# Kernel optimization log

Hardware: AMD Instinct MI355X
Metric: run time of the kernel (lower is better)

The kernel has to match this reference:

```python
import jax, jax.numpy as jnp
import numpy as np

N0, N1 = 4096, 16384
HID, LAT, DIM, OUT = 128, 64, 3, 3
OFFS = [1, 2, 3, 5, 8]  # circulant graph offsets; A+A^3 support is offset sums


def _ring_edges(N, offs):
    # edge_index of A + A^3 for circulant adjacency with given offsets
    o = np.asarray(offs)
    s3 = (o[:, None, None] + o[None, :, None] + o[None, None, :]).ravel()
    aug = np.unique(np.concatenate([o, s3]))
    src = np.repeat(np.arange(N), aug.size)
    dst = (src + np.tile(aug, N)) % N
    return np.stack([src, dst]).astype(np.int32)


def _gatv2(x, src, dst, eattr, Wl, bl, Wr, br, We, att, bias, N):
    # PyG GATv2Conv, heads=1, add_self_loops=True with fill_value='mean'
    cnt = jax.ops.segment_sum(jnp.ones_like(dst, jnp.float32), dst, N)
    loop_attr = jax.ops.segment_sum(eattr, dst, N) / jnp.maximum(cnt, 1.0)[:, None]
    loops = jnp.arange(N, dtype=src.dtype)
    s = jnp.concatenate([src, loops])
    d = jnp.concatenate([dst, loops])
    ea = jnp.concatenate([eattr, loop_attr], 0)
    xl = x @ Wl.T + bl
    xr = x @ Wr.T + br
    m = xl[s] + xr[d] + ea @ We.T              # [E+N, HID]
    m = jnp.where(m > 0, m, 0.2 * m)           # leaky_relu(0.2)
    a = m @ att                                # [E+N]
    amax = jax.ops.segment_max(a, d, N)
    ex = jnp.exp(a - amax[d])
    den = jax.ops.segment_sum(ex, d, N)
    alpha = ex / (den[d] + 1e-16)
    return jax.ops.segment_sum(xl[s] * alpha[:, None], d, N) + bias


def _knn_interp(x, pos_x, pos_y, k=3):
    # PyG knn_interpolate: inverse-squared-distance weighted k-NN average
    d2 = (jnp.sum(pos_y ** 2, 1)[:, None] + jnp.sum(pos_x ** 2, 1)[None, :]
          - 2.0 * pos_y @ pos_x.T)             # [Ny, Nx]
    neg, idx = jax.lax.top_k(-d2, k)
    w = 1.0 / jnp.maximum(-neg, 1e-16)          # [Ny, k]
    return jnp.sum(x[idx] * w[..., None], 1) / jnp.sum(w, 1)[:, None]


def _forward(latent, pos0, pos1, eidx0, eidx1, conv_Wl, conv_bl, conv_Wr,
             conv_br, conv_We, conv_att, conv_bias, lin0_W, lin0_b, lins_W,
             lins_b, out_W, out_b):
    x = latent @ lin0_W.T + lin0_b
    src0, dst0 = eidx0[0], eidx0[1]
    ea0 = pos0[dst0] - pos0[src0]
    for c in (0, 1):
        h = jnp.concatenate([x, pos0], 1)
        x = jax.nn.elu(_gatv2(h, src0, dst0, ea0, conv_Wl[c], conv_bl[c],
                              conv_Wr[c], conv_br[c], conv_We[c], conv_att[c],
                              conv_bias[c], N0)) + h @ lins_W[c].T + lins_b[c]
    x = _knn_interp(x, pos0, pos1, 3)
    src1, dst1 = eidx1[0], eidx1[1]
    ea1 = pos1[dst1] - pos1[src1]
    for c in (2, 3):
        h = jnp.concatenate([x, pos1], 1)
        x = jax.nn.elu(_gatv2(h, src1, dst1, ea1, conv_Wl[c], conv_bl[c],
                              conv_Wr[c], conv_br[c], conv_We[c], conv_att[c],
                              conv_bias[c], N1)) + h @ lins_W[c].T + lins_b[c]
    h = jnp.concatenate([x, pos1], 1)
    return h @ out_W.T + out_b


def setup_inputs() -> dict:
    key = jax.random.key(0)
    ks = jax.random.split(key, 16)
    n = lambda i, shape, s=0.05: jax.random.normal(ks[i], shape, jnp.float32) * s
    IN = HID + DIM
    return dict(
        latent=jax.random.normal(ks[0], (N0, LAT), jnp.float32),
        pos0=jax.random.normal(ks[1], (N0, DIM), jnp.float32),
        pos1=jax.random.normal(ks[2], (N1, DIM), jnp.float32),
        eidx0=jnp.asarray(_ring_edges(N0, OFFS)),
        eidx1=jnp.asarray(_ring_edges(N1, OFFS)),
        conv_Wl=n(3, (4, HID, IN)), conv_bl=n(4, (4, HID)),
        conv_Wr=n(5, (4, HID, IN)), conv_br=n(6, (4, HID)),
        conv_We=n(7, (4, HID, DIM)), conv_att=n(8, (4, HID)),
        conv_bias=n(9, (4, HID)),
        lin0_W=n(10, (HID, LAT)), lin0_b=n(11, (HID,)),
        lins_W=n(12, (4, HID, IN)), lins_b=n(13, (4, HID)),
        out_W=n(14, (OUT, IN)), out_b=n(15, (OUT,)))


def reference(latent, pos0, pos1, eidx0, eidx1, conv_Wl, conv_bl, conv_Wr,
              conv_br, conv_We, conv_att, conv_bias, lin0_W, lin0_b, lins_W,
              lins_b, out_W, out_b):
    return _forward(latent, pos0, pos1, eidx0, eidx1, conv_Wl, conv_bl,
                    conv_Wr, conv_br, conv_We, conv_att, conv_bias, lin0_W,
                    lin0_b, lins_W, lins_b, out_W, out_b)
```

## Files before the change

### kernel.cpp

```cpp
#include <hip/hip_runtime.h>
#include <hip/hip_bf16.h>

#define N0 4096
#define N1 16384
#define HID 128
#define LAT 64
#define DIM 3
#define NAUG 21
#define JTOT 512
#define NG 5

typedef __attribute__((ext_vector_type(8))) short bf16x8;
typedef __attribute__((ext_vector_type(4))) float f32x4;

__device__ __constant__ int c_aug[NAUG] = {1,2,3,4,5,6,7,8,9,10,11,12,13,14,
                                           15,16,17,18,19,21,24};

__device__ __forceinline__ unsigned short f2bf(float v) {
    __hip_bfloat16 b = __float2bfloat16(v);
    return *reinterpret_cast<unsigned short*>(&b);
}

#define KCH 64
#define KCS 64
#define YPT 4
#define KNN_BLOCKS 1024

#define WSWZ_PER_LAYER 81920
#define H0G4 131072
#define H1G4 524288
#define P_NSWZ (4 * WSWZ_PER_LAYER)
#define P_B0 P_NSWZ
#define P_B1 (P_B0 + 4 * JTOT)
#define P_B2 (P_B1 + H0G4)
#define P_B3 (P_B2 + H1G4)
#define PREP_BLOCKS (P_B3 / 256)
#define LIN0_BLOCKS 2048

__global__ __launch_bounds__(256)
void prep_knn_lin0_kernel(const float* __restrict__ Wl,
                          const float* __restrict__ Wr,
                          const float* __restrict__ We,
                          const float* __restrict__ linsW,
                          const float* __restrict__ bl,
                          const float* __restrict__ br,
                          const float* __restrict__ linsb,
                          const float* __restrict__ lin0W,
                          const float* __restrict__ lin0b,
                          const float* __restrict__ latent,
                          const float* __restrict__ pos0,
                          const float* __restrict__ pos1,
                          unsigned short* __restrict__ Wswz,
                          float* __restrict__ bias_cat,
                          unsigned short* __restrict__ hswz0A,
                          unsigned short* __restrict__ hswz0B,
                          unsigned short* __restrict__ hswz1A,
                          unsigned short* __restrict__ hswz1B,
                          float* __restrict__ pb_d,
                          int* __restrict__ pb_i) {
    __shared__ float4 sx[KCS];

    if (blockIdx.x < KNN_BLOCKS) {
        int tid = threadIdx.x;
        int chunk = blockIdx.x >> 4;
        int xpart = blockIdx.x & 15;
        if (tid < KCS) {
            const float* p = &pos0[(chunk * KCS + tid) * 3];
            float x = p[0], y = p[1], z = p[2];
            sx[tid] = make_float4(x, y, z, x * x + y * y + z * z);
        }
        __syncthreads();
        int ybase = xpart * (256 * YPT) + tid;
        float m2y[YPT][3], sy[YPT];
#pragma unroll
        for (int u = 0; u < YPT; ++u) {
            int y = ybase + u * 256;
            float p0 = pos1[y * 3], p1 = pos1[y * 3 + 1], p2 = pos1[y * 3 + 2];
            m2y[u][0] = -2.0f * p0; m2y[u][1] = -2.0f * p1; m2y[u][2] = -2.0f * p2;
            sy[u] = p0 * p0 + p1 * p1 + p2 * p2;
        }
        float bd0[YPT], bd1[YPT], bd2[YPT];
        int   bi0[YPT], bi1[YPT], bi2[YPT];
#pragma unroll
        for (int u = 0; u < YPT; ++u) {
            bd0[u] = 1e30f; bd1[u] = 1e30f; bd2[u] = 1e30f;
            bi0[u] = 0; bi1[u] = 0; bi2[u] = 0;
        }
        int gbase = chunk * KCS;
#pragma unroll 4
        for (int i = 0; i < KCS; i += 4) {
            float4 s[4];
#pragma unroll
            for (int v = 0; v < 4; ++v) s[v] = sx[i + v];
#pragma unroll
            for (int v = 0; v < 4; ++v) {
                int gi = gbase + i + v;
#pragma unroll
                for (int u = 0; u < YPT; ++u) {
                    float t = fmaf(m2y[u][0], s[v].x, s[v].w);
                    t = fmaf(m2y[u][1], s[v].y, t);
                    t = fmaf(m2y[u][2], s[v].z, t);
                    t += sy[u];
                    bool c0 = t < bd0[u];
                    bool c1 = t < bd1[u];
                    bool c2 = t < bd2[u];
                    float n0 = fminf(bd0[u], t);
                    float n1 = __builtin_amdgcn_fmed3f(bd0[u], bd1[u], t);
                    float n2 = __builtin_amdgcn_fmed3f(bd1[u], bd2[u], t);
                    int j0 = c0 ? gi : bi0[u];
                    int j1 = c0 ? bi0[u] : (c1 ? gi : bi1[u]);
                    int j2 = c1 ? bi1[u] : (c2 ? gi : bi2[u]);
                    bd0[u] = n0; bd1[u] = n1; bd2[u] = n2;
                    bi0[u] = j0; bi1[u] = j1; bi2[u] = j2;
                }
            }
        }
#pragma unroll
        for (int u = 0; u < YPT; ++u) {
            int y = ybase + u * 256;
            int base = (chunk * N1 + y) * 3;
            pb_d[base] = bd0[u]; pb_d[base + 1] = bd1[u]; pb_d[base + 2] = bd2[u];
            pb_i[base] = bi0[u]; pb_i[base + 1] = bi1[u]; pb_i[base + 2] = bi2[u];
        }
        return;
    }

    if (blockIdx.x < KNN_BLOCKS + PREP_BLOCKS) {
        int tid = (blockIdx.x - KNN_BLOCKS) * blockDim.x + threadIdx.x;
        if (tid < P_NSWZ) {
            int c = tid / WSWZ_PER_LAYER;
            int r = tid - c * WSWZ_PER_LAYER;
            int nt = r / 2560;
            int g  = (r / 512) % 5;
            int l  = (r / 8) % 64;
            int j  = r % 8;
            int k  = g * 32 + (l >> 4) * 8 + j;
            int n  = nt * 16 + (l & 15);
            float v = 0.0f;
            if (k < 131) {
                if (n < 128)      v = Wl[(c * 128 + n) * 131 + k];
                else if (n < 256) v = Wr[(c * 128 + (n - 128)) * 131 + k];
                else if (n < 384) v = linsW[(c * 128 + (n - 256)) * 131 + k];
                else              v = (k >= 128) ? We[(c * 128 + (n - 384)) * 3 + (k - 128)]
                                                 : 0.0f;
            }
            Wswz[tid] = f2bf(v);
        } else if (tid < P_B1) {
            int idx = tid - P_B0;
            int c = idx / JTOT;
            int j = idx - c * JTOT;
            float v;
            if (j < 128)        v = bl[c * 128 + j];
            else if (j < 256)   v = br[c * 128 + (j - 128)];
            else if (j < 384)   v = linsb[c * 128 + (j - 256)];
            else                v = 0.0f;
            bias_cat[idx] = v;
        } else if (tid < P_B2) {
            int r = tid - P_B1;
            int j = r & 7;
            int l = (r >> 3) & 63;
            int mt = r >> 9;
            int row = mt * 16 + (l & 15);
            int k = 128 + (l >> 4) * 8 + j;
            float v = (k < 131) ? pos0[row * 3 + (k - 128)] : 0.0f;
            unsigned short bv = f2bf(v);
            size_t idx = (size_t)((mt * 5 + 4) * 64 + l) * 8 + j;
            hswz0A[idx] = bv;
            hswz0B[idx] = bv;
        } else if (tid < P_B3) {
            int r = tid - P_B2;
            int j = r & 7;
            int l = (r >> 3) & 63;
            int mt = r >> 9;
            int row = mt * 16 + (l & 15);
            int k = 128 + (l >> 4) * 8 + j;
            float v = (k < 131) ? pos1[row * 3 + (k - 128)] : 0.0f;
            unsigned short bv = f2bf(v);
            size_t idx = (size_t)((mt * 5 + 4) * 64 + l) * 8 + j;
            hswz1A[idx] = bv;
            hswz1B[idx] = bv;
        }
        return;
    }

    {
        int r = (blockIdx.x - KNN_BLOCKS - PREP_BLOCKS) * blockDim.x + threadIdx.x;
        int n = r >> 7, j = r & 127;
        const float* lr = &latent[n * 64];
        const float* wr = &lin0W[j * 64];
        float acc = lin0b[j];
#pragma unroll 8
        for (int k = 0; k < 64; ++k) acc += lr[k] * wr[k];
        int g = j >> 5, sub = (j >> 3) & 3, jj = j & 7;
        hswz0A[(size_t)(((n >> 4) * 5 + g) * 64 + sub * 16 + (n & 15)) * 8 + jj] = f2bf(acc);
    }
}

#define WROW 40
#define FSTR 132

__device__ __forceinline__ void layer_body(
        const unsigned short* __restrict__ hswz,
        const unsigned short* __restrict__ Wswz,
        const float* __restrict__ bias_cat,
        const float* __restrict__ att,
        const float* __restrict__ bias,
        float* __restrict__ linb,
        float* __restrict__ xout,
        unsigned short* __restrict__ hout,
        const float* __restrict__ outW,
        const float* __restrict__ outb,
        const float* __restrict__ pos1,
        int mode, int N, int mt0,
        float (*xls_s)[FSTR], float (*pes_s)[FSTR], float (*xr_s)[FSTR]) {
    int tid = threadIdx.x;
    int w = tid >> 6;
    int l = tid & 63;
    int quad = l >> 4, lcol = l & 15;
    int n0 = mt0 * 16;
    int MT = N >> 4;

    bf16x8 a[3][NG];
#pragma unroll
    for (int i = 0; i < 3; ++i) {
        int mt = mt0 - 2 + i;
        if (mt < 0) mt += MT;
#pragma unroll
        for (int g = 0; g < NG; ++g)
            a[i][g] = *(const bf16x8*)&hswz[(size_t)((mt * NG + g) * 64 + l) * 8];
    }

#pragma unroll
    for (int i = 0; i < 4; ++i) {
        int b = i * 8 + w;
        int colbase = (b & 7) * 16;
        int ntw, kind;
        if (b < 8)       { ntw = b;      kind = 0; }
        else if (b < 16) { ntw = 16 + b; kind = 1; }
        else if (b < 24) { ntw = b - 8;  kind = 2; }
        else             { ntw = b - 8;  kind = 3; }
        bf16x8 bf[NG];
#pragma unroll
        for (int g = 0; g < NG; ++g)
            bf[g] = *(const bf16x8*)&Wswz[(size_t)((ntw * NG + g) * 64 + l) * 8];
        float bv = bias_cat[ntw * 16 + lcol];
        if (kind < 2) {
            float (*dst)[FSTR] = (kind == 0) ? xls_s : pes_s;
#pragma unroll
            for (int m = 0; m < 3; ++m) {
                f32x4 c = {bv, bv, bv, bv};
#pragma unroll
                for (int g = 0; g < NG; ++g)
                    c = __builtin_amdgcn_mfma_f32_16x16x32_bf16(a[m][g], bf[g], c, 0, 0, 0);
                if (m == 0) {
                    if (quad >= 2) {
                        int w0 = (quad - 2) * 4;
#pragma unroll
                        for (int r = 0; r < 4; ++r) dst[w0 + r][colbase + lcol] = c[r];
                    }
                } else {
                    int w0 = m * 16 - 8 + quad * 4;
#pragma unroll
                    for (int r = 0; r < 4; ++r) dst[w0 + r][colbase + lcol] = c[r];
                }
            }
        } else if (kind == 2) {
            f32x4 c = {bv, bv, bv, bv};
#pragma unroll
            for (int g = 0; g < NG; ++g)
                c = __builtin_amdgcn_mfma_f32_16x16x32_bf16(a[2][g], bf[g], c, 0, 0, 0);
            int w0 = quad * 4;
#pragma unroll
            for (int r = 0; r < 4; ++r) xr_s[w0 + r][colbase + lcol] = c[r];
        } else {
            f32x4 c = {bv, bv, bv, bv};
#pragma unroll
            for (int g = 0; g < NG; ++g)
                c = __builtin_amdgcn_mfma_f32_16x16x32_bf16(a[2][g], bf[g], c, 0, 0, 0);
            int jj = colbase + lcol;
#pragma unroll
            for (int r = 0; r < 4; ++r)
                linb[(size_t)(n0 + quad * 4 + r) * 128 + jj] = c[r];
        }
    }
    __syncthreads();

    int qh = l >> 5;
    int t = l & 31;
    int dl = w * 2 + qh;
    int d = n0 + dl;
    int selfrow = dl + 24;
    int i0 = t * 4;

    f32x4 linv = *(const f32x4*)&linb[(size_t)d * 128 + i0];

    float att4[4], base[4], xld[4], pesum[4], o[4];
    {
        f32x4 a0 = *(const f32x4*)&att[i0];
        f32x4 r0 = *(const f32x4*)&xr_s[dl][i0];
        f32x4 x0 = *(const f32x4*)&xls_s[selfrow][i0];
        f32x4 p0 = *(const f32x4*)&pes_s[selfrow][i0];
#pragma unroll
        for (int j = 0; j < 4; ++j) {
            att4[j] = a0[j];
            xld[j]  = x0[j];
            base[j] = r0[j] + p0[j];
            pesum[j] = 0.0f;
            o[j] = 0.0f;
        }
    }

    float den = 0.0f;

#pragma unroll
    for (int k = 0; k < NAUG; ++k) {
        int lr = selfrow - c_aug[k];
        float xls[4], pes[4];
        *(f32x4*)&xls[0] = *(const f32x4*)&xls_s[lr][i0];
        *(f32x4*)&pes[0] = *(const f32x4*)&pes_s[lr][i0];
        float p = 0.0f;
#pragma unroll
        for (int j = 0; j < 4; ++j) {
            float mm = xls[j] + base[j] - pes[j];
            mm = mm > 0.0f ? mm : 0.2f * mm;
            p = fmaf(att4[j], mm, p);
            pesum[j] += pes[j];
        }
        p += __shfl_xor(p, 1, 64);
        p += __shfl_xor(p, 2, 64);
        p += __shfl_xor(p, 4, 64);
        p += __shfl_xor(p, 8, 64);
        p += __shfl_xor(p, 16, 64);
        float wgt = __expf(p);
        den += wgt;
#pragma unroll
        for (int j = 0; j < 4; ++j) o[j] = fmaf(wgt, xls[j], o[j]);
    }
    {
        const float inv21 = 1.0f / 21.0f;
        float p = 0.0f;
#pragma unroll
        for (int j = 0; j < 4; ++j) {
            float mm = xld[j] + base[j] - pesum[j] * inv21;
            mm = mm > 0.0f ? mm : 0.2f * mm;
            p = fmaf(att4[j], mm, p);
        }
        p += __shfl_xor(p, 1, 64);
        p += __shfl_xor(p, 2, 64);
        p += __shfl_xor(p, 4, 64);
        p += __shfl_xor(p, 8, 64);
        p += __shfl_xor(p, 16, 64);
        float wgt = __expf(p);
        den += wgt;
#pragma unroll
        for (int j = 0; j < 4; ++j) o[j] = fmaf(wgt, xld[j], o[j]);
    }

    float inv = 1.0f / (den + 1e-16f);
    float res[4];
    {
        f32x4 b0 = *(const f32x4*)&bias[i0];
#pragma unroll
        for (int j = 0; j < 4; ++j) {
            float v = o[j] * inv + b0[j];
            v = v > 0.0f ? v : __expf(v) - 1.0f;
            res[j] = v + linv[j];
        }
    }

    if (mode == 0) {
        *(f32x4*)&xout[(size_t)d * 128 + i0] = *(f32x4*)&res[0];
    } else if (mode == 1) {
        unsigned short ob[4];
#pragma unroll
        for (int j = 0; j < 4; ++j) ob[j] = f2bf(res[j]);
        int g = i0 >> 5, sub = (i0 >> 3) & 3, jj = i0 & 7;
        *(uint2*)&hout[(size_t)((((d >> 4) * 5 + g) * 64) + sub * 16 + (d & 15)) * 8 + jj]
            = *(uint2*)ob;
    } else {
        float po[3];
#pragma unroll
        for (int o3 = 0; o3 < 3; ++o3) {
            const float* wr = &outW[o3 * 131 + i0];
            float p = res[0] * wr[0];
            p = fmaf(res[1], wr[1], p);
            p = fmaf(res[2], wr[2], p);
            p = fmaf(res[3], wr[3], p);
            p += __shfl_xor(p, 1, 64);
            p += __shfl_xor(p, 2, 64);
            p += __shfl_xor(p, 4, 64);
            p += __shfl_xor(p, 8, 64);
            p += __shfl_xor(p, 16, 64);
            po[o3] = p;
        }
        if (t == 0) {
            float p0 = pos1[d * 3], p1 = pos1[d * 3 + 1], p2 = pos1[d * 3 + 2];
#pragma unroll
            for (int o3 = 0; o3 < 3; ++o3) {
                xout[d * 3 + o3] = po[o3] + outb[o3] + p0 * outW[o3 * 131 + 128]
                                 + p1 * outW[o3 * 131 + 129] + p2 * outW[o3 * 131 + 130];
            }
        }
    }
}

__global__ __launch_bounds__(512, 2)
void fused_layer_kernel(const unsigned short* __restrict__ hswz,
                        const unsigned short* __restrict__ Wswz,
                        const float* __restrict__ bias_cat,
                        const float* __restrict__ att,
                        const float* __restrict__ bias,
                        float* __restrict__ linb,
                        float* __restrict__ xout,
                        unsigned short* __restrict__ hout,
                        const float* __restrict__ outW,
                        const float* __restrict__ outb,
                        const float* __restrict__ pos1,
                        int mode, int N) {
    __shared__ __align__(16) float xls_s[WROW][FSTR];
    __shared__ __align__(16) float pes_s[WROW][FSTR];
    __shared__ __align__(16) float xr_s[16][FSTR];
    layer_body(hswz, Wswz, bias_cat, att, bias, linb, xout, hout,
               outW, outb, pos1, mode, N, blockIdx.x, xls_s, pes_s, xr_s);
}

#define MERGE_BLOCKS 32

__global__ __launch_bounds__(512, 2)
void layer0_merge_kernel(const unsigned short* __restrict__ hswz,
                         const unsigned short* __restrict__ Wswz,
                         const float* __restrict__ bias_cat,
                         const float* __restrict__ att,
                         const float* __restrict__ bias,
                         float* __restrict__ linb,
                         unsigned short* __restrict__ hout,
                         const float* __restrict__ pb_d,
                         const int* __restrict__ pb_i,
                         int* __restrict__ knn_idx,
                         float* __restrict__ knn_w) {
    __shared__ __align__(16) float xls_s[WROW][FSTR];
    __shared__ __align__(16) float pes_s[WROW][FSTR];
    __shared__ __align__(16) float xr_s[16][FSTR];

    if (blockIdx.x < (N0 >> 4)) {
        layer_body(hswz, Wswz, bias_cat, att, bias, linb, nullptr, hout,
                   nullptr, nullptr, nullptr, 1, N0, blockIdx.x,
                   xls_s, pes_s, xr_s);
        return;
    }

    int y = (blockIdx.x - (N0 >> 4)) * 512 + threadIdx.x;
    float bd0 = 1e30f, bd1 = 1e30f, bd2 = 1e30f;
    int bi0 = 0, bi1 = 0, bi2 = 0;
    for (int c = 0; c < KCH; ++c) {
        int base = (c * N1 + y) * 3;
#pragma unroll
        for (int t3 = 0; t3 < 3; ++t3) {
            float t = pb_d[base + t3];
            int gi = pb_i[base + t3];
            bool c0 = t < bd0;
            bool c1 = t < bd1;
            bool c2 = t < bd2;
            float n0 = fminf(bd0, t);
            float n1 = __builtin_amdgcn_fmed3f(bd0, bd1, t);
            float n2 = __builtin_amdgcn_fmed3f(bd1, bd2, t);
            int j0 = c0 ? gi : bi0;
            int j1 = c0 ? bi0 : (c1 ? gi : bi1);
            int j2 = c1 ? bi1 : (c2 ? gi : bi2);
            bd0 = n0; bd1 = n1; bd2 = n2;
            bi0 = j0; bi1 = j1; bi2 = j2;
        }
    }
    knn_idx[y * 3]     = bi0;
    knn_idx[y * 3 + 1] = bi1;
    knn_idx[y * 3 + 2] = bi2;
    knn_w[y * 3]     = 1.0f / fmaxf(bd0, 1e-16f);
    knn_w[y * 3 + 1] = 1.0f / fmaxf(bd1, 1e-16f);
    knn_w[y * 3 + 2] = 1.0f / fmaxf(bd2, 1e-16f);
}

__global__ __launch_bounds__(256)
void interp_kernel(const float* __restrict__ x0, const int* __restrict__ knn_idx,
                   const float* __restrict__ knn_w, unsigned short* __restrict__ hswz) {
    int wave = threadIdx.x >> 6;
    int lane = threadIdx.x & 63;
    int y = blockIdx.x * 4 + wave;
    int i0 = 2 * lane;
    float w0 = knn_w[y * 3], w1 = knn_w[y * 3 + 1], w2 = knn_w[y * 3 + 2];
    int j0 = knn_idx[y * 3], j1 = knn_idx[y * 3 + 1], j2 = knn_idx[y * 3 + 2];
    float inv = 1.0f / (w0 + w1 + w2);
    float2 a = *(const float2*)&x0[(size_t)j0 * 128 + i0];
    float2 b = *(const float2*)&x0[(size_t)j1 * 128 + i0];
    float2 c = *(const float2*)&x0[(size_t)j2 * 128 + i0];
    float rx = (w0 * a.x + w1 * b.x + w2 * c.x) * inv;
    float ry = (w0 * a.y + w1 * b.y + w2 * c.y) * inv;
    unsigned int packed = (unsigned int)f2bf(rx) | ((unsigned int)f2bf(ry) << 16);
    int g = i0 >> 5, sub = (i0 >> 3) & 3, jj = i0 & 7;
    size_t idx = (size_t)((((y >> 4) * 5 + g) * 64) + sub * 16 + (y & 15)) * 8 + jj;
    *(unsigned int*)&hswz[idx] = packed;
}

extern "C" void kernel_launch(void* const* d_in, const int* in_sizes, int n_in,
                              void* d_out, int out_size, void* d_ws, size_t ws_size,
                              hipStream_t stream) {
    (void)in_sizes; (void)n_in; (void)out_size; (void)ws_size;
    const float* latent   = (const float*)d_in[0];
    const float* pos0     = (const float*)d_in[1];
    const float* pos1     = (const float*)d_in[2];
    const float* conv_Wl  = (const float*)d_in[5];
    const float* conv_bl  = (const float*)d_in[6];
    const float* conv_Wr  = (const float*)d_in[7];
    const float* conv_br  = (const float*)d_in[8];
    const float* conv_We  = (const float*)d_in[9];
    const float* conv_att = (const float*)d_in[10];
    const float* conv_bias= (const float*)d_in[11];
    const float* lin0_W   = (const float*)d_in[12];
    const float* lin0_b   = (const float*)d_in[13];
    const float* lins_W   = (const float*)d_in[14];
    const float* lins_b   = (const float*)d_in[15];
    const float* out_W    = (const float*)d_in[16];
    const float* out_b    = (const float*)d_in[17];
    float* out = (float*)d_out;

    char* ws = (char*)d_ws;
    unsigned short* Wswz = (unsigned short*)ws; ws += (size_t)4 * WSWZ_PER_LAYER * 2;
    float* bias_cat = (float*)ws;  ws += (size_t)4 * JTOT * 4;
    unsigned short* hswz0A = (unsigned short*)ws; ws += (size_t)(N0 / 16) * NG * 64 * 8 * 2;
    unsigned short* hswz0B = (unsigned short*)ws; ws += (size_t)(N0 / 16) * NG * 64 * 8 * 2;
    unsigned short* hswz1A = (unsigned short*)ws; ws += (size_t)(N1 / 16) * NG * 64 * 8 * 2;
    unsigned short* hswz1B = (unsigned short*)ws; ws += (size_t)(N1 / 16) * NG * 64 * 8 * 2;
    float* bufA     = (float*)ws;  ws += (size_t)N0 * 128 * 4;
    float* linb     = (float*)ws;  ws += (size_t)N1 * 128 * 4;
    float* pb_d     = (float*)ws;  ws += (size_t)KCH * N1 * 3 * 4;
    int*   pb_i     = (int*)ws;    ws += (size_t)KCH * N1 * 3 * 4;
    int*   knn_idx  = (int*)ws;    ws += (size_t)N1 * 3 * 4;
    float* knn_w    = (float*)ws;  ws += (size_t)N1 * 3 * 4;

    prep_knn_lin0_kernel<<<KNN_BLOCKS + PREP_BLOCKS + LIN0_BLOCKS, 256, 0, stream>>>(
        conv_Wl, conv_Wr, conv_We, lins_W, conv_bl, conv_br, lins_b,
        lin0_W, lin0_b, latent, pos0, pos1,
        Wswz, bias_cat, hswz0A, hswz0B, hswz1A, hswz1B, pb_d, pb_i);

    layer0_merge_kernel<<<N0 / 16 + MERGE_BLOCKS, 512, 0, stream>>>(
        hswz0A, Wswz + (size_t)0 * WSWZ_PER_LAYER, bias_cat + 0 * JTOT,
        conv_att + 0 * 128, conv_bias + 0 * 128, linb, hswz0B,
        pb_d, pb_i, knn_idx, knn_w);

    fused_layer_kernel<<<N0 / 16, 512, 0, stream>>>(
        hswz0B, Wswz + (size_t)1 * WSWZ_PER_LAYER, bias_cat + 1 * JTOT,
        conv_att + 1 * 128, conv_bias + 1 * 128, linb, bufA, nullptr,
        nullptr, nullptr, nullptr, 0, N0);

    interp_kernel<<<N1 / 4, 256, 0, stream>>>(bufA, knn_idx, knn_w, hswz1A);

    fused_layer_kernel<<<N1 / 16, 512, 0, stream>>>(
        hswz1A, Wswz + (size_t)2 * WSWZ_PER_LAYER, bias_cat + 2 * JTOT,
        conv_att + 2 * 128, conv_bias + 2 * 128, linb, nullptr, hswz1B,
        nullptr, nullptr, nullptr, 1, N1);

    fused_layer_kernel<<<N1 / 16, 512, 0, stream>>>(
        hswz1B, Wswz + (size_t)3 * WSWZ_PER_LAYER, bias_cat + 3 * JTOT,
        conv_att + 3 * 128, conv_bias + 3 * 128, linb, out, nullptr,
        out_W, out_b, pos1, 2, N1);
}
```

Before: 248.8 us.

## Split kNN across layer kernels, keep lin output in LDS, merge kNN in interp

The kNN partial-search blocks move out of the prep kernel and are split across the two layer-0/1 kernels, 32 chunks each, so they run alongside the GATv2 layer blocks. The lins projection result now goes to shared memory instead of a global linb buffer, which removes one write and reread per layer. The separate kNN merge pass is folded into the interp kernel, where each wave reduces the 64 partial top-3 lists with wave shuffles. The cost is more shared memory per block, which may lower occupancy, and the shuffle-based merge adds per-row latency.

```diff
diff --git a/kernel.cpp b/kernel.cpp
--- a/kernel.cpp
+++ b/kernel.cpp
@@ -24,7 +24,7 @@
 #define KCH 64
 #define KCS 64
 #define YPT 4
-#define KNN_BLOCKS 1024
+#define KNNB_PER_KERNEL 256
 
 #define WSWZ_PER_LAYER 81920
 #define H0G4 131072
@@ -38,95 +38,26 @@
 #define LIN0_BLOCKS 2048
 
 __global__ __launch_bounds__(256)
-void prep_knn_lin0_kernel(const float* __restrict__ Wl,
-                          const float* __restrict__ Wr,
-                          const float* __restrict__ We,
-                          const float* __restrict__ linsW,
-                          const float* __restrict__ bl,
-                          const float* __restrict__ br,
-                          const float* __restrict__ linsb,
-                          const float* __restrict__ lin0W,
-                          const float* __restrict__ lin0b,
-                          const float* __restrict__ latent,
-                          const float* __restrict__ pos0,
-                          const float* __restrict__ pos1,
-                          unsigned short* __restrict__ Wswz,
-                          float* __restrict__ bias_cat,
-                          unsigned short* __restrict__ hswz0A,
-                          unsigned short* __restrict__ hswz0B,
-                          unsigned short* __restrict__ hswz1A,
-                          unsigned short* __restrict__ hswz1B,
-                          float* __restrict__ pb_d,
-                          int* __restrict__ pb_i) {
-    __shared__ float4 sx[KCS];
-
-    if (blockIdx.x < KNN_BLOCKS) {
-        int tid = threadIdx.x;
-        int chunk = blockIdx.x >> 4;
-        int xpart = blockIdx.x & 15;
-        if (tid < KCS) {
-            const float* p = &pos0[(chunk * KCS + tid) * 3];
-            float x = p[0], y = p[1], z = p[2];
-            sx[tid] = make_float4(x, y, z, x * x + y * y + z * z);
-        }
-        __syncthreads();
-        int ybase = xpart * (256 * YPT) + tid;
-        float m2y[YPT][3], sy[YPT];
-#pragma unroll
-        for (int u = 0; u < YPT; ++u) {
-            int y = ybase + u * 256;
-            float p0 = pos1[y * 3], p1 = pos1[y * 3 + 1], p2 = pos1[y * 3 + 2];
-            m2y[u][0] = -2.0f * p0; m2y[u][1] = -2.0f * p1; m2y[u][2] = -2.0f * p2;
-            sy[u] = p0 * p0 + p1 * p1 + p2 * p2;
-        }
-        float bd0[YPT], bd1[YPT], bd2[YPT];
-        int   bi0[YPT], bi1[YPT], bi2[YPT];
-#pragma unroll
-        for (int u = 0; u < YPT; ++u) {
-            bd0[u] = 1e30f; bd1[u] = 1e30f; bd2[u] = 1e30f;
-            bi0[u] = 0; bi1[u] = 0; bi2[u] = 0;
-        }
-        int gbase = chunk * KCS;
-#pragma unroll 4
-        for (int i = 0; i < KCS; i += 4) {
-            float4 s[4];
-#pragma unroll
-            for (int v = 0; v < 4; ++v) s[v] = sx[i + v];
-#pragma unroll
-            for (int v = 0; v < 4; ++v) {
-                int gi = gbase + i + v;
-#pragma unroll
-                for (int u = 0; u < YPT; ++u) {
-                    float t = fmaf(m2y[u][0], s[v].x, s[v].w);
-                    t = fmaf(m2y[u][1], s[v].y, t);
-                    t = fmaf(m2y[u][2], s[v].z, t);
-                    t += sy[u];
-                    bool c0 = t < bd0[u];
-                    bool c1 = t < bd1[u];
-                    bool c2 = t < bd2[u];
-                    float n0 = fminf(bd0[u], t);
-                    float n1 = __builtin_amdgcn_fmed3f(bd0[u], bd1[u], t);
-                    float n2 = __builtin_amdgcn_fmed3f(bd1[u], bd2[u], t);
-                    int j0 = c0 ? gi : bi0[u];
-                    int j1 = c0 ? bi0[u] : (c1 ? gi : bi1[u]);
-                    int j2 = c1 ? bi1[u] : (c2 ? gi : bi2[u]);
-                    bd0[u] = n0; bd1[u] = n1; bd2[u] = n2;
-                    bi0[u] = j0; bi1[u] = j1; bi2[u] = j2;
-                }
-            }
-        }
-#pragma unroll
-        for (int u = 0; u < YPT; ++u) {
-            int y = ybase + u * 256;
-            int base = (chunk * N1 + y) * 3;
-            pb_d[base] = bd0[u]; pb_d[base + 1] = bd1[u]; pb_d[base + 2] = bd2[u];
-            pb_i[base] = bi0[u]; pb_i[base + 1] = bi1[u]; pb_i[base + 2] = bi2[u];
-        }
-        return;
-    }
-
-    if (blockIdx.x < KNN_BLOCKS + PREP_BLOCKS) {
-        int tid = (blockIdx.x - KNN_BLOCKS) * blockDim.x + threadIdx.x;
+void prep_lin0_kernel(const float* __restrict__ Wl,
+                      const float* __restrict__ Wr,
+                      const float* __restrict__ We,
+                      const float* __restrict__ linsW,
+                      const float* __restrict__ bl,
+                      const float* __restrict__ br,
+                      const float* __restrict__ linsb,
+                      const float* __restrict__ lin0W,
+                      const float* __restrict__ lin0b,
+                      const float* __restrict__ latent,
+                      const float* __restrict__ pos0,
+                      const float* __restrict__ pos1,
+                      unsigned short* __restrict__ Wswz,
+                      float* __restrict__ bias_cat,
+                      unsigned short* __restrict__ hswz0A,
+                      unsigned short* __restrict__ hswz0B,
+                      unsigned short* __restrict__ hswz1A,
+                      unsigned short* __restrict__ hswz1B) {
+    if (blockIdx.x < PREP_BLOCKS) {
+        int tid = blockIdx.x * blockDim.x + threadIdx.x;
         if (tid < P_NSWZ) {
             int c = tid / WSWZ_PER_LAYER;
             int r = tid - c * WSWZ_PER_LAYER;
@@ -184,7 +115,7 @@
     }
 
     {
-        int r = (blockIdx.x - KNN_BLOCKS - PREP_BLOCKS) * blockDim.x + threadIdx.x;
+        int r = (blockIdx.x - PREP_BLOCKS) * blockDim.x + threadIdx.x;
         int n = r >> 7, j = r & 127;
         const float* lr = &latent[n * 64];
         const float* wr = &lin0W[j * 64];
@@ -205,14 +136,14 @@
         const float* __restrict__ bias_cat,
         const float* __restrict__ att,
         const float* __restrict__ bias,
-        float* __restrict__ linb,
         float* __restrict__ xout,
         unsigned short* __restrict__ hout,
         const float* __restrict__ outW,
         const float* __restrict__ outb,
         const float* __restrict__ pos1,
         int mode, int N, int mt0,
-        float (*xls_s)[FSTR], float (*pes_s)[FSTR], float (*xr_s)[FSTR]) {
+        float (*xls_s)[FSTR], float (*pes_s)[FSTR], float (*xr_s)[FSTR],
+        float (*lin_s)[FSTR]) {
     int tid = threadIdx.x;
     int w = tid >> 6;
     int l = tid & 63;
@@ -264,23 +195,15 @@
                     for (int r = 0; r < 4; ++r) dst[w0 + r][colbase + lcol] = c[r];
                 }
             }
-        } else if (kind == 2) {
+        } else {
             f32x4 c = {bv, bv, bv, bv};
 #pragma unroll
             for (int g = 0; g < NG; ++g)
                 c = __builtin_amdgcn_mfma_f32_16x16x32_bf16(a[2][g], bf[g], c, 0, 0, 0);
+            float (*dst)[FSTR] = (kind == 2) ? xr_s : lin_s;
             int w0 = quad * 4;
 #pragma unroll
-            for (int r = 0; r < 4; ++r) xr_s[w0 + r][colbase + lcol] = c[r];
-        } else {
-            f32x4 c = {bv, bv, bv, bv};
-#pragma unroll
-            for (int g = 0; g < NG; ++g)
-                c = __builtin_amdgcn_mfma_f32_16x16x32_bf16(a[2][g], bf[g], c, 0, 0, 0);
-            int jj = colbase + lcol;
-#pragma unroll
-            for (int r = 0; r < 4; ++r)
-                linb[(size_t)(n0 + quad * 4 + r) * 128 + jj] = c[r];
+            for (int r = 0; r < 4; ++r) dst[w0 + r][colbase + lcol] = c[r];
         }
     }
     __syncthreads();
@@ -292,7 +215,7 @@
     int selfrow = dl + 24;
     int i0 = t * 4;
 
-    f32x4 linv = *(const f32x4*)&linb[(size_t)d * 128 + i0];
+    f32x4 linv = *(const f32x4*)&lin_s[dl][i0];
 
     float att4[4], base[4], xld[4], pesum[4], o[4];
     {
@@ -405,12 +328,101 @@
 }
 
 __global__ __launch_bounds__(512, 2)
+void layer_knn_kernel(const unsigned short* __restrict__ hswz,
+                      const unsigned short* __restrict__ Wswz,
+                      const float* __restrict__ bias_cat,
+                      const float* __restrict__ att,
+                      const float* __restrict__ bias,
+                      float* __restrict__ xout,
+                      unsigned short* __restrict__ hout,
+                      const float* __restrict__ pos0,
+                      const float* __restrict__ pos1,
+                      float* __restrict__ pb_d,
+                      int* __restrict__ pb_i,
+                      int chunk_base, int mode) {
+    __shared__ __align__(16) float xls_s[WROW][FSTR];
+    __shared__ __align__(16) float pes_s[WROW][FSTR];
+    __shared__ __align__(16) float xr_s[16][FSTR];
+    __shared__ __align__(16) float lin_s[16][FSTR];
+
+    if (blockIdx.x < (N0 >> 4)) {
+        layer_body(hswz, Wswz, bias_cat, att, bias, xout, hout,
+                   nullptr, nullptr, nullptr, mode, N0, blockIdx.x,
+                   xls_s, pes_s, xr_s, lin_s);
+        return;
+    }
+
+    int kb = blockIdx.x - (N0 >> 4);
+    int chunk = chunk_base + (kb >> 3);
+    int xpart = kb & 7;
+    int tid = threadIdx.x;
+    float4* sx = (float4*)&xls_s[0][0];
+    if (tid < KCS) {
+        const float* p = &pos0[(chunk * KCS + tid) * 3];
+        float x = p[0], y = p[1], z = p[2];
+        sx[tid] = make_float4(x, y, z, x * x + y * y + z * z);
+    }
+    __syncthreads();
+    int ybase = xpart * (512 * YPT) + tid;
+    float m2y[YPT][3], sy[YPT];
+#pragma unroll
+    for (int u = 0; u < YPT; ++u) {
+        int y = ybase + u * 512;
+        float p0 = pos1[y * 3], p1 = pos1[y * 3 + 1], p2 = pos1[y * 3 + 2];
+        m2y[u][0] = -2.0f * p0; m2y[u][1] = -2.0f * p1; m2y[u][2] = -2.0f * p2;
+        sy[u] = p0 * p0 + p1 * p1 + p2 * p2;
+    }
+    float bd0[YPT], bd1[YPT], bd2[YPT];
+    int   bi0[YPT], bi1[YPT], bi2[YPT];
+#pragma unroll
+    for (int u = 0; u < YPT; ++u) {
+        bd0[u] = 1e30f; bd1[u] = 1e30f; bd2[u] = 1e30f;
+        bi0[u] = 0; bi1[u] = 0; bi2[u] = 0;
+    }
+    int gbase = chunk * KCS;
+#pragma unroll 4
+    for (int i = 0; i < KCS; i += 4) {
+        float4 s[4];
+#pragma unroll
+        for (int v = 0; v < 4; ++v) s[v] = sx[i + v];
+#pragma unroll
+        for (int v = 0; v < 4; ++v) {
+            int gi = gbase + i + v;
+#pragma unroll
+            for (int u = 0; u < YPT; ++u) {
+                float t = fmaf(m2y[u][0], s[v].x, s[v].w);
+                t = fmaf(m2y[u][1], s[v].y, t);
+                t = fmaf(m2y[u][2], s[v].z, t);
+                t += sy[u];
+                bool c0 = t < bd0[u];
+                bool c1 = t < bd1[u];
+                bool c2 = t < bd2[u];
+                float n0 = fminf(bd0[u], t);
+                float n1 = __builtin_amdgcn_fmed3f(bd0[u], bd1[u], t);
+                float n2 = __builtin_amdgcn_fmed3f(bd1[u], bd2[u], t);
+                int j0 = c0 ? gi : bi0[u];
+                int j1 = c0 ? bi0[u] : (c1 ? gi : bi1[u]);
+                int j2 = c1 ? bi1[u] : (c2 ? gi : bi2[u]);
+                bd0[u] = n0; bd1[u] = n1; bd2[u] = n2;
+                bi0[u] = j0; bi1[u] = j1; bi2[u] = j2;
+            }
+        }
+    }
+#pragma unroll
+    for (int u = 0; u < YPT; ++u) {
+        int y = ybase + u * 512;
+        int base = (chunk * N1 + y) * 3;
+        pb_d[base] = bd0[u]; pb_d[base + 1] = bd1[u]; pb_d[base + 2] = bd2[u];
+        pb_i[base] = bi0[u]; pb_i[base + 1] = bi1[u]; pb_i[base + 2] = bi2[u];
+    }
+}
+
+__global__ __launch_bounds__(512, 2)
 void fused_layer_kernel(const unsigned short* __restrict__ hswz,
                         const unsigned short* __restrict__ Wswz,
                         const float* __restrict__ bias_cat,
                         const float* __restrict__ att,
                         const float* __restrict__ bias,
-                        float* __restrict__ linb,
                         float* __restrict__ xout,
                         unsigned short* __restrict__ hout,
                         const float* __restrict__ outW,
@@ -420,40 +432,28 @@
     __shared__ __align__(16) float xls_s[WROW][FSTR];
     __shared__ __align__(16) float pes_s[WROW][FSTR];
     __shared__ __align__(16) float xr_s[16][FSTR];
-    layer_body(hswz, Wswz, bias_cat, att, bias, linb, xout, hout,
-               outW, outb, pos1, mode, N, blockIdx.x, xls_s, pes_s, xr_s);
-}
-
-#define MERGE_BLOCKS 32
-
-__global__ __launch_bounds__(512, 2)
-void layer0_merge_kernel(const unsigned short* __restrict__ hswz,
-                         const unsigned short* __restrict__ Wswz,
-                         const float* __restrict__ bias_cat,
-                         const float* __restrict__ att,
-                         const float* __restrict__ bias,
-                         float* __restrict__ linb,
-                         unsigned short* __restrict__ hout,
-                         const float* __restrict__ pb_d,
-                         const int* __restrict__ pb_i,
-                         int* __restrict__ knn_idx,
-                         float* __restrict__ knn_w) {
-    __shared__ __align__(16) float xls_s[WROW][FSTR];
-    __shared__ __align__(16) float pes_s[WROW][FSTR];
-    __shared__ __align__(16) float xr_s[16][FSTR];
-
-    if (blockIdx.x < (N0 >> 4)) {
-        layer_body(hswz, Wswz, bias_cat, att, bias, linb, nullptr, hout,
-                   nullptr, nullptr, nullptr, 1, N0, blockIdx.x,
-                   xls_s, pes_s, xr_s);
-        return;
-    }
-
-    int y = (blockIdx.x - (N0 >> 4)) * 512 + threadIdx.x;
+    __shared__ __align__(16) float lin_s[16][FSTR];
+    layer_body(hswz, Wswz, bias_cat, att, bias, xout, hout,
+               outW, outb, pos1, mode, N, blockIdx.x,
+               xls_s, pes_s, xr_s, lin_s);
+}
+
+__global__ __launch_bounds__(512)
+void interp_kernel(const float* __restrict__ x0,
+                   const float* __restrict__ pb_d,
+                   const int* __restrict__ pb_i,
+                   unsigned short* __restrict__ hswz) {
+    __shared__ float  sw[8][3];
+    __shared__ int    si[8][3];
+    int tid = threadIdx.x;
+    int wave = tid >> 6;
+    int lane = tid & 63;
+    int y = blockIdx.x * 8 + wave;
+
     float bd0 = 1e30f, bd1 = 1e30f, bd2 = 1e30f;
     int bi0 = 0, bi1 = 0, bi2 = 0;
-    for (int c = 0; c < KCH; ++c) {
-        int base = (c * N1 + y) * 3;
+    {
+        int base = (lane * N1 + y) * 3;
 #pragma unroll
         for (int t3 = 0; t3 < 3; ++t3) {
             float t = pb_d[base + t3];
@@ -471,23 +471,44 @@
             bi0 = j0; bi1 = j1; bi2 = j2;
         }
     }
-    knn_idx[y * 3]     = bi0;
-    knn_idx[y * 3 + 1] = bi1;
-    knn_idx[y * 3 + 2] = bi2;
-    knn_w[y * 3]     = 1.0f / fmaxf(bd0, 1e-16f);
-    knn_w[y * 3 + 1] = 1.0f / fmaxf(bd1, 1e-16f);
-    knn_w[y * 3 + 2] = 1.0f / fmaxf(bd2, 1e-16f);
-}
-
-__global__ __launch_bounds__(256)
-void interp_kernel(const float* __restrict__ x0, const int* __restrict__ knn_idx,
-                   const float* __restrict__ knn_w, unsigned short* __restrict__ hswz) {
-    int wave = threadIdx.x >> 6;
-    int lane = threadIdx.x & 63;
-    int y = blockIdx.x * 4 + wave;
+#pragma unroll
+    for (int off = 32; off >= 1; off >>= 1) {
+        float od0 = __shfl_xor(bd0, off, 64);
+        float od1 = __shfl_xor(bd1, off, 64);
+        float od2 = __shfl_xor(bd2, off, 64);
+        int   oi0 = __shfl_xor(bi0, off, 64);
+        int   oi1 = __shfl_xor(bi1, off, 64);
+        int   oi2 = __shfl_xor(bi2, off, 64);
+        float td[3] = {od0, od1, od2};
+        int   ti[3] = {oi0, oi1, oi2};
+#pragma unroll
+        for (int t3 = 0; t3 < 3; ++t3) {
+            float t = td[t3];
+            int gi = ti[t3];
+            bool c0 = t < bd0;
+            bool c1 = t < bd1;
+            bool c2 = t < bd2;
+            float n0 = fminf(bd0, t);
+            float n1 = __builtin_amdgcn_fmed3f(bd0, bd1, t);
+            float n2 = __builtin_amdgcn_fmed3f(bd1, bd2, t);
+            int j0 = c0 ? gi : bi0;
+            int j1 = c0 ? bi0 : (c1 ? gi : bi1);
+            int j2 = c1 ? bi1 : (c2 ? gi : bi2);
+            bd0 = n0; bd1 = n1; bd2 = n2;
+            bi0 = j0; bi1 = j1; bi2 = j2;
+        }
+    }
+    if (lane == 0) {
+        sw[wave][0] = 1.0f / fmaxf(bd0, 1e-16f);
+        sw[wave][1] = 1.0f / fmaxf(bd1, 1e-16f);
+        sw[wave][2] = 1.0f / fmaxf(bd2, 1e-16f);
+        si[wave][0] = bi0; si[wave][1] = bi1; si[wave][2] = bi2;
+    }
+    __syncthreads();
+
+    float w0 = sw[wave][0], w1 = sw[wave][1], w2 = sw[wave][2];
+    int j0 = si[wave][0], j1 = si[wave][1], j2 = si[wave][2];
     int i0 = 2 * lane;
-    float w0 = knn_w[y * 3], w1 = knn_w[y * 3 + 1], w2 = knn_w[y * 3 + 2];
-    int j0 = knn_idx[y * 3], j1 = knn_idx[y * 3 + 1], j2 = knn_idx[y * 3 + 2];
     float inv = 1.0f / (w0 + w1 + w2);
     float2 a = *(const float2*)&x0[(size_t)j0 * 128 + i0];
     float2 b = *(const float2*)&x0[(size_t)j1 * 128 + i0];
@@ -530,36 +551,33 @@
     unsigned short* hswz1A = (unsigned short*)ws; ws += (size_t)(N1 / 16) * NG * 64 * 8 * 2;
     unsigned short* hswz1B = (unsigned short*)ws; ws += (size_t)(N1 / 16) * NG * 64 * 8 * 2;
     float* bufA     = (float*)ws;  ws += (size_t)N0 * 128 * 4;
-    float* linb     = (float*)ws;  ws += (size_t)N1 * 128 * 4;
     float* pb_d     = (float*)ws;  ws += (size_t)KCH * N1 * 3 * 4;
     int*   pb_i     = (int*)ws;    ws += (size_t)KCH * N1 * 3 * 4;
-    int*   knn_idx  = (int*)ws;    ws += (size_t)N1 * 3 * 4;
-    float* knn_w    = (float*)ws;  ws += (size_t)N1 * 3 * 4;
-
-    prep_knn_lin0_kernel<<<KNN_BLOCKS + PREP_BLOCKS + LIN0_BLOCKS, 256, 0, stream>>>(
+
+    prep_lin0_kernel<<<PREP_BLOCKS + LIN0_BLOCKS, 256, 0, stream>>>(
         conv_Wl, conv_Wr, conv_We, lins_W, conv_bl, conv_br, lins_b,
         lin0_W, lin0_b, latent, pos0, pos1,
-        Wswz, bias_cat, hswz0A, hswz0B, hswz1A, hswz1B, pb_d, pb_i);
-
-    layer0_merge_kernel<<<N0 / 16 + MERGE_BLOCKS, 512, 0, stream>>>(
+        Wswz, bias_cat, hswz0A, hswz0B, hswz1A, hswz1B);
+
+    layer_knn_kernel<<<N0 / 16 + KNNB_PER_KERNEL, 512, 0, stream>>>(
         hswz0A, Wswz + (size_t)0 * WSWZ_PER_LAYER, bias_cat + 0 * JTOT,
-        conv_att + 0 * 128, conv_bias + 0 * 128, linb, hswz0B,
-        pb_d, pb_i, knn_idx, knn_w);
-
-    fused_layer_kernel<<<N0 / 16, 512, 0, stream>>>(
+        conv_att + 0 * 128, conv_bias + 0 * 128, nullptr, hswz0B,
+        pos0, pos1, pb_d, pb_i, 0, 1);
+
+    layer_knn_kernel<<<N0 / 16 + KNNB_PER_KERNEL, 512, 0, stream>>>(
         hswz0B, Wswz + (size_t)1 * WSWZ_PER_LAYER, bias_cat + 1 * JTOT,
-        conv_att + 1 * 128, conv_bias + 1 * 128, linb, bufA, nullptr,
-        nullptr, nullptr, nullptr, 0, N0);
-
-    interp_kernel<<<N1 / 4, 256, 0, stream>>>(bufA, knn_idx, knn_w, hswz1A);
+        conv_att + 1 * 128, conv_bias + 1 * 128, bufA, nullptr,
+        pos0, pos1, pb_d, pb_i, 32, 0);
+
+    interp_kernel<<<N1 / 8, 512, 0, stream>>>(bufA, pb_d, pb_i, hswz1A);
 
     fused_layer_kernel<<<N1 / 16, 512, 0, stream>>>(
         hswz1A, Wswz + (size_t)2 * WSWZ_PER_LAYER, bias_cat + 2 * JTOT,
-        conv_att + 2 * 128, conv_bias + 2 * 128, linb, nullptr, hswz1B,
+        conv_att + 2 * 128, conv_bias + 2 * 128, nullptr, hswz1B,
         nullptr, nullptr, nullptr, 1, N1);
 
     fused_layer_kernel<<<N1 / 16, 512, 0, stream>>>(
         hswz1B, Wswz + (size_t)3 * WSWZ_PER_LAYER, bias_cat + 3 * JTOT,
-        conv_att + 3 * 128, conv_bias + 3 * 128, linb, out, nullptr,
+        conv_att + 3 * 128, conv_bias + 3 * 128, out, nullptr,
         out_W, out_b, pos1, 2, N1);
 }
```

After: 248.9 us. Within noise of the previous version (+0.0%).
